# Kernel tuning notes

Hardware: AMD Instinct MI355X
Metric: run time of the kernel (lower is better)

## Reference

```python
import jax, jax.numpy as jnp
import numpy as np

B = 1024            # batch
F = (16, 16, 16)    # factors (f1, f2, f3)
BOND = 32           # bond dimension
SIZE = 4096         # prod(F)


def setup_inputs() -> dict:
    key = jax.random.key(0)
    k0, k1, k2, k3 = jax.random.split(key, 4)
    x = jax.random.normal(k0, (B, SIZE), dtype=jnp.float32)
    # cores: (r_{k-1}, f_k, f_k, r_k), boundary ranks = 1, init scale 0.01 as in torch
    core0 = jax.random.normal(k1, (1, F[0], F[0], BOND), dtype=jnp.float32) * 0.01
    core1 = jax.random.normal(k2, (BOND, F[1], F[1], BOND), dtype=jnp.float32) * 0.01
    core2 = jax.random.normal(k3, (BOND, F[2], F[2], 1), dtype=jnp.float32) * 0.01
    bias = jnp.zeros((SIZE,), dtype=jnp.float32)
    return {"x": x, "core0": core0, "core1": core1, "core2": core2, "bias": bias}


def reference(x, core0, core1, core2, bias):
    # Batched MPO (tensor-train) matvec: y[b, i1 i2 i3] = sum_{j1 j2 j3, r1 r2}
    #   G0[1, i1, j1, r1] G1[r1, i2, j2, r2] G2[r2, i3, j3, 1] * x[b, j1 j2 j3]
    b = x.shape[0]
    t = x.reshape(b, F[0], F[1], F[2])                       # (B, j1, j2, j3)
    # contract j1 with core0 -> carry bond r, accumulate output index i1 at the end
    t = jnp.einsum('bjkl,aijr->brkli', t, core0)             # (B, r1, j2, j3, i1)
    # contract (r1, j2) with core1
    t = jnp.einsum('brkli,rmks->bslim', t, core1)            # (B, r2, j3, i1, i2)
    # contract (r2, j3) with core2 (right bond t has size 1)
    y = jnp.einsum('bslim,snlt->bimnt', t, core2)            # (B, i1, i2, i3, 1)
    return y.reshape(b, SIZE) + bias
```

## Files before the change

### kernel.cpp

```cpp
#include <hip/hip_runtime.h>
#include <stdint.h>

typedef float f32x4_t __attribute__((ext_vector_type(4)));
typedef __bf16 bf16x8_t __attribute__((ext_vector_type(8)));

#define GLD16(gp, lp) __builtin_amdgcn_global_load_lds( \
    (const __attribute__((address_space(1))) void*)(gp), \
    (__attribute__((address_space(3))) void*)(lp), 16, 0, 0)

__device__ __forceinline__ uint32_t f2bf(float f) {
  uint32_t u = __float_as_uint(f);
  u += 0x7FFFu + ((u >> 16) & 1u);
  return u >> 16;
}
__device__ __forceinline__ uint32_t pack2(float a, float b) {
  return f2bf(a) | (f2bf(b) << 16);
}

__global__ __launch_bounds__(256) void build_m01_kernel(
    const float* __restrict__ c0, const float* __restrict__ c1,
    float* __restrict__ M01) {
  const int a = blockIdx.x, t = threadIdx.x;
  const int i1 = a >> 4, i2 = a & 15, j1 = t >> 4, j2 = t & 15;
  const float* c0p = c0 + (i1 * 16 + j1) * 32;
  const float4* c1v = (const float4*)(c1 + i2 * 512 + j2 * 32);

  float acc[32];
  #pragma unroll
  for (int r2 = 0; r2 < 32; ++r2) acc[r2] = 0.f;

  #pragma unroll 4
  for (int r1 = 0; r1 < 32; ++r1) {
    const float g = c0p[r1];
    #pragma unroll
    for (int q = 0; q < 8; ++q) {
      const float4 v = c1v[r1 * 2048 + q];
      acc[q * 4 + 0] += g * v.x; acc[q * 4 + 1] += g * v.y;
      acc[q * 4 + 2] += g * v.z; acc[q * 4 + 3] += g * v.w;
    }
  }
  float4* dst = (float4*)(M01 + (size_t)a * 8192 + t * 32);
  #pragma unroll
  for (int q = 0; q < 8; ++q) {
    float4 v = {acc[q * 4 + 0], acc[q * 4 + 1], acc[q * 4 + 2], acc[q * 4 + 3]};
    dst[q] = v;
  }
}

__global__ __launch_bounds__(256) void build_w2_kernel(
    const float* __restrict__ M01, const float* __restrict__ c2,
    uint16_t* __restrict__ W) {
  __shared__ float C2L[32 * 16];
  const int bid = blockIdx.x;
  const int a = bid >> 4, i3 = bid & 15, t = threadIdx.x;

  if (t < 128) {
    ((float4*)C2L)[t] = ((const float4*)c2)[(t >> 2) * 64 + i3 * 4 + (t & 3)];
  }
  __syncthreads();

  float M[32];
  const float4* mp = (const float4*)(M01 + (size_t)a * 8192 + t * 32);
  #pragma unroll
  for (int q = 0; q < 8; ++q) {
    const float4 v = mp[q];
    M[q * 4 + 0] = v.x; M[q * 4 + 1] = v.y; M[q * 4 + 2] = v.z; M[q * 4 + 3] = v.w;
  }

  float acc[16];
  #pragma unroll
  for (int j = 0; j < 16; ++j) acc[j] = 0.f;

  #pragma unroll 4
  for (int r2 = 0; r2 < 32; ++r2) {
    const float4* cp = (const float4*)(C2L + r2 * 16);
    const float4 q0 = cp[0], q1 = cp[1], q2 = cp[2], q3 = cp[3];
    const float m = M[r2];
    acc[0]  += m * q0.x; acc[1]  += m * q0.y; acc[2]  += m * q0.z; acc[3]  += m * q0.w;
    acc[4]  += m * q1.x; acc[5]  += m * q1.y; acc[6]  += m * q1.z; acc[7]  += m * q1.w;
    acc[8]  += m * q2.x; acc[9]  += m * q2.y; acc[10] += m * q2.z; acc[11] += m * q2.w;
    acc[12] += m * q3.x; acc[13] += m * q3.y; acc[14] += m * q3.z; acc[15] += m * q3.w;
  }

  uint4 o0, o1;
  o0.x = pack2(acc[0],  acc[1]);  o0.y = pack2(acc[2],  acc[3]);
  o0.z = pack2(acc[4],  acc[5]);  o0.w = pack2(acc[6],  acc[7]);
  o1.x = pack2(acc[8],  acc[9]);  o1.y = pack2(acc[10], acc[11]);
  o1.z = pack2(acc[12], acc[13]); o1.w = pack2(acc[14], acc[15]);
  uint4* dst = (uint4*)(W + (size_t)(a * 16 + i3) * 4096 + t * 16);
  dst[0] = o0; dst[1] = o1;
}

__global__ __launch_bounds__(256) void cvt_x_kernel(const float* __restrict__ x,
                                                    uint32_t* __restrict__ xb) {
  const int i = blockIdx.x * 256 + threadIdx.x;
  const float4* x4 = (const float4*)x;
  const float4 a = x4[2 * i], b = x4[2 * i + 1];
  uint4 o;
  o.x = pack2(a.x, a.y); o.y = pack2(a.z, a.w);
  o.z = pack2(b.x, b.y); o.w = pack2(b.z, b.w);
  ((uint4*)xb)[i] = o;
}

__global__ __launch_bounds__(256, 2) void gemm_bt_bias_kernel(
    const uint16_t* __restrict__ A, const uint16_t* __restrict__ Bt,
    const float* __restrict__ bias, float* __restrict__ C) {
  constexpr int Kd = 4096, Nd = 4096;
  __shared__ uint16_t As[2][64 * 64];
  __shared__ uint16_t Bs[2][128 * 64];
  const int t = threadIdx.x;
  const int wid = t >> 6, lane = t & 63;

  const int bid = blockIdx.x;
  const int g = bid & 7, idx = bid >> 3;
  const int ntile = g * 4 + (idx >> 4);
  const int mtile = idx & 15;
  const int brow = mtile * 64, bcol = ntile * 128;

  const uint16_t* Ab = A + (size_t)brow * Kd;
  const uint16_t* Bb = Bt + (size_t)bcol * Kd;

  const int rb = t >> 3;
  const int ce = ((t & 7) * 8) ^ ((rb & 7) << 3);
  const uint16_t* gA = Ab + (size_t)rb * Kd + ce;
  const uint16_t* gB = Bb + (size_t)rb * Kd + ce;
  const int wofs = wid * 512;

  const int wm = wid >> 1, wn = wid & 1;
  const int fr = lane & 15, fk = (lane >> 4) * 8;
  const int csw = (fr & 7) << 3;

  f32x4_t zero = {0.f, 0.f, 0.f, 0.f};
  f32x4_t acc[2][4];
  #pragma unroll
  for (int m = 0; m < 2; ++m)
    #pragma unroll
    for (int n = 0; n < 4; ++n) acc[m][n] = zero;

  #define STAGE(buf, kt)                                             \
    do {                                                             \
      GLD16(gA + (kt), As[buf] + wofs);                              \
      GLD16(gA + (size_t)32 * Kd + (kt), As[buf] + 2048 + wofs);     \
      GLD16(gB + (kt), Bs[buf] + wofs);                              \
      GLD16(gB + (size_t)32 * Kd + (kt), Bs[buf] + 2048 + wofs);     \
      GLD16(gB + (size_t)64 * Kd + (kt), Bs[buf] + 4096 + wofs);     \
      GLD16(gB + (size_t)96 * Kd + (kt), Bs[buf] + 6144 + wofs);     \
    } while (0)

  STAGE(0, 0);
  __syncthreads();

  int cur = 0;
  for (int kt = 0; kt < Kd; kt += 64) {
    if (kt + 64 < Kd) STAGE(cur ^ 1, kt + 64);

    bf16x8_t af[2][2], bfr[2][4];
    #pragma unroll
    for (int kk = 0; kk < 2; ++kk) {
      const int col = (kk * 32 + fk) ^ csw;
      #pragma unroll
      for (int m = 0; m < 2; ++m)
        af[kk][m] = *(const bf16x8_t*)(As[cur] + (wm * 32 + m * 16 + fr) * 64 + col);
      #pragma unroll
      for (int n = 0; n < 4; ++n)
        bfr[kk][n] = *(const bf16x8_t*)(Bs[cur] + (wn * 64 + n * 16 + fr) * 64 + col);
    }
    #pragma unroll
    for (int kk = 0; kk < 2; ++kk)
      #pragma unroll
      for (int m = 0; m < 2; ++m)
        #pragma unroll
        for (int n = 0; n < 4; ++n)
          acc[m][n] = __builtin_amdgcn_mfma_f32_16x16x32_bf16(
              af[kk][m], bfr[kk][n], acc[m][n], 0, 0, 0);

    __syncthreads();
    cur ^= 1;
  }
  #undef STAGE

  const int orow = brow + wm * 32 + (lane >> 4) * 4;
  const int ocol = bcol + wn * 64 + fr;
  #pragma unroll
  for (int n = 0; n < 4; ++n) {
    const float bv = bias[ocol + n * 16];
    #pragma unroll
    for (int m = 0; m < 2; ++m) {
      float* Cp = C + (size_t)(orow + m * 16) * Nd + ocol + n * 16;
      #pragma unroll
      for (int r = 0; r < 4; ++r) Cp[(size_t)r * Nd] = acc[m][n][r] + bv;
    }
  }
}

extern "C" void kernel_launch(void* const* d_in, const int* in_sizes, int n_in,
                              void* d_out, int out_size, void* d_ws, size_t ws_size,
                              hipStream_t stream) {
  const float* x    = (const float*)d_in[0];
  const float* c0   = (const float*)d_in[1];
  const float* c1   = (const float*)d_in[2];
  const float* c2   = (const float*)d_in[3];
  const float* bias = (const float*)d_in[4];
  float* y = (float*)d_out;

  uint16_t* W   = (uint16_t*)d_ws;
  char*     slab = (char*)d_ws + (size_t)4096 * 4096 * 2;
  float*    M01 = (float*)slab;
  uint16_t* xb  = (uint16_t*)slab;

  build_m01_kernel<<<256, 256, 0, stream>>>(c0, c1, M01);
  build_w2_kernel<<<4096, 256, 0, stream>>>(M01, c2, W);
  cvt_x_kernel<<<2048, 256, 0, stream>>>(x, (uint32_t*)xb);
  gemm_bt_bias_kernel<<<512, 256, 0, stream>>>(xb, W, bias, y);
}
```

Before: 192.0 us.

## Single-buffer GEMM LDS staging and batch four i3 slices per W-build block

The GEMM drops its double-buffered LDS pipeline. It now loads each K tile into a single buffer and waits on a barrier before the MFMAs, which halves LDS use and may raise occupancy, but it no longer overlaps global loads with compute. The W-build kernel now has each block handle four i3 slices, so M01 rows are read once per four outputs instead of once per output. Block indices are also remapped with an XCD-style interleave.

Result: faster. 182.4 us (-5.0%).

```diff
diff --git a/kernel.cpp b/kernel.cpp
--- a/kernel.cpp
+++ b/kernel.cpp
@@ -50,12 +50,19 @@
 __global__ __launch_bounds__(256) void build_w2_kernel(
     const float* __restrict__ M01, const float* __restrict__ c2,
     uint16_t* __restrict__ W) {
-  __shared__ float C2L[32 * 16];
-  const int bid = blockIdx.x;
-  const int a = bid >> 4, i3 = bid & 15, t = threadIdx.x;
-
-  if (t < 128) {
-    ((float4*)C2L)[t] = ((const float4*)c2)[(t >> 2) * 64 + i3 * 4 + (t & 3)];
+  __shared__ float C2L[4][512];
+  const int bid0 = blockIdx.x;
+  const int bid = (bid0 & 7) * 128 + (bid0 >> 3);
+  const int a = bid >> 2, i3q = (bid & 3) << 2;
+  const int t = threadIdx.x;
+
+  #pragma unroll
+  for (int s = 0; s < 2; ++s) {
+    const int idx = t * 2 + s;
+    const int sl = idx >> 7;
+    const int rem = idx & 127;
+    ((float4*)C2L[sl])[rem] =
+        ((const float4*)c2)[(rem >> 2) * 64 + (i3q + sl) * 4 + (rem & 3)];
   }
   __syncthreads();
 
@@ -67,28 +74,32 @@
     M[q * 4 + 0] = v.x; M[q * 4 + 1] = v.y; M[q * 4 + 2] = v.z; M[q * 4 + 3] = v.w;
   }
 
-  float acc[16];
-  #pragma unroll
-  for (int j = 0; j < 16; ++j) acc[j] = 0.f;
-
-  #pragma unroll 4
-  for (int r2 = 0; r2 < 32; ++r2) {
-    const float4* cp = (const float4*)(C2L + r2 * 16);
-    const float4 q0 = cp[0], q1 = cp[1], q2 = cp[2], q3 = cp[3];
-    const float m = M[r2];
-    acc[0]  += m * q0.x; acc[1]  += m * q0.y; acc[2]  += m * q0.z; acc[3]  += m * q0.w;
-    acc[4]  += m * q1.x; acc[5]  += m * q1.y; acc[6]  += m * q1.z; acc[7]  += m * q1.w;
-    acc[8]  += m * q2.x; acc[9]  += m * q2.y; acc[10] += m * q2.z; acc[11] += m * q2.w;
-    acc[12] += m * q3.x; acc[13] += m * q3.y; acc[14] += m * q3.z; acc[15] += m * q3.w;
-  }
-
-  uint4 o0, o1;
-  o0.x = pack2(acc[0],  acc[1]);  o0.y = pack2(acc[2],  acc[3]);
-  o0.z = pack2(acc[4],  acc[5]);  o0.w = pack2(acc[6],  acc[7]);
-  o1.x = pack2(acc[8],  acc[9]);  o1.y = pack2(acc[10], acc[11]);
-  o1.z = pack2(acc[12], acc[13]); o1.w = pack2(acc[14], acc[15]);
-  uint4* dst = (uint4*)(W + (size_t)(a * 16 + i3) * 4096 + t * 16);
-  dst[0] = o0; dst[1] = o1;
+  #pragma unroll 1
+  for (int i3l = 0; i3l < 4; ++i3l) {
+    float acc[16];
+    #pragma unroll
+    for (int j = 0; j < 16; ++j) acc[j] = 0.f;
+
+    const float* C2s = C2L[i3l];
+    #pragma unroll 4
+    for (int r2 = 0; r2 < 32; ++r2) {
+      const float4* cp = (const float4*)(C2s + r2 * 16);
+      const float4 q0 = cp[0], q1 = cp[1], q2 = cp[2], q3 = cp[3];
+      const float m = M[r2];
+      acc[0]  += m * q0.x; acc[1]  += m * q0.y; acc[2]  += m * q0.z; acc[3]  += m * q0.w;
+      acc[4]  += m * q1.x; acc[5]  += m * q1.y; acc[6]  += m * q1.z; acc[7]  += m * q1.w;
+      acc[8]  += m * q2.x; acc[9]  += m * q2.y; acc[10] += m * q2.z; acc[11] += m * q2.w;
+      acc[12] += m * q3.x; acc[13] += m * q3.y; acc[14] += m * q3.z; acc[15] += m * q3.w;
+    }
+
+    uint4 o0, o1;
+    o0.x = pack2(acc[0],  acc[1]);  o0.y = pack2(acc[2],  acc[3]);
+    o0.z = pack2(acc[4],  acc[5]);  o0.w = pack2(acc[6],  acc[7]);
+    o1.x = pack2(acc[8],  acc[9]);  o1.y = pack2(acc[10], acc[11]);
+    o1.z = pack2(acc[12], acc[13]); o1.w = pack2(acc[14], acc[15]);
+    uint4* dst = (uint4*)(W + (size_t)(a * 16 + i3q + i3l) * 4096 + t * 16);
+    dst[0] = o0; dst[1] = o1;
+  }
 }
 
 __global__ __launch_bounds__(256) void cvt_x_kernel(const float* __restrict__ x,
@@ -106,8 +117,8 @@
     const uint16_t* __restrict__ A, const uint16_t* __restrict__ Bt,
     const float* __restrict__ bias, float* __restrict__ C) {
   constexpr int Kd = 4096, Nd = 4096;
-  __shared__ uint16_t As[2][64 * 64];
-  __shared__ uint16_t Bs[2][128 * 64];
+  __shared__ uint16_t As[64 * 64];
+  __shared__ uint16_t Bs[128 * 64];
   const int t = threadIdx.x;
   const int wid = t >> 6, lane = t & 63;
 
@@ -124,7 +135,12 @@
   const int ce = ((t & 7) * 8) ^ ((rb & 7) << 3);
   const uint16_t* gA = Ab + (size_t)rb * Kd + ce;
   const uint16_t* gB = Bb + (size_t)rb * Kd + ce;
-  const int wofs = wid * 512;
+  uint16_t* lA0 = As + wid * 512;
+  uint16_t* lA1 = As + 2048 + wid * 512;
+  uint16_t* lB0 = Bs + wid * 512;
+  uint16_t* lB1 = Bs + 2048 + wid * 512;
+  uint16_t* lB2 = Bs + 4096 + wid * 512;
+  uint16_t* lB3 = Bs + 6144 + wid * 512;
 
   const int wm = wid >> 1, wn = wid & 1;
   const int fr = lane & 15, fk = (lane >> 4) * 8;
@@ -137,22 +153,14 @@
     #pragma unroll
     for (int n = 0; n < 4; ++n) acc[m][n] = zero;
 
-  #define STAGE(buf, kt)                                             \
-    do {                                                             \
-      GLD16(gA + (kt), As[buf] + wofs);                              \
-      GLD16(gA + (size_t)32 * Kd + (kt), As[buf] + 2048 + wofs);     \
-      GLD16(gB + (kt), Bs[buf] + wofs);                              \
-      GLD16(gB + (size_t)32 * Kd + (kt), Bs[buf] + 2048 + wofs);     \
-      GLD16(gB + (size_t)64 * Kd + (kt), Bs[buf] + 4096 + wofs);     \
-      GLD16(gB + (size_t)96 * Kd + (kt), Bs[buf] + 6144 + wofs);     \
-    } while (0)
-
-  STAGE(0, 0);
-  __syncthreads();
-
-  int cur = 0;
   for (int kt = 0; kt < Kd; kt += 64) {
-    if (kt + 64 < Kd) STAGE(cur ^ 1, kt + 64);
+    GLD16(gA + kt, lA0);
+    GLD16(gA + (size_t)32 * Kd + kt, lA1);
+    GLD16(gB + kt, lB0);
+    GLD16(gB + (size_t)32 * Kd + kt, lB1);
+    GLD16(gB + (size_t)64 * Kd + kt, lB2);
+    GLD16(gB + (size_t)96 * Kd + kt, lB3);
+    __syncthreads();
 
     bf16x8_t af[2][2], bfr[2][4];
     #pragma unroll
@@ -160,10 +168,10 @@
       const int col = (kk * 32 + fk) ^ csw;
       #pragma unroll
       for (int m = 0; m < 2; ++m)
-        af[kk][m] = *(const bf16x8_t*)(As[cur] + (wm * 32 + m * 16 + fr) * 64 + col);
+        af[kk][m] = *(const bf16x8_t*)(As + (wm * 32 + m * 16 + fr) * 64 + col);
       #pragma unroll
       for (int n = 0; n < 4; ++n)
-        bfr[kk][n] = *(const bf16x8_t*)(Bs[cur] + (wn * 64 + n * 16 + fr) * 64 + col);
+        bfr[kk][n] = *(const bf16x8_t*)(Bs + (wn * 64 + n * 16 + fr) * 64 + col);
     }
     #pragma unroll
     for (int kk = 0; kk < 2; ++kk)
@@ -173,11 +181,8 @@
         for (int n = 0; n < 4; ++n)
           acc[m][n] = __builtin_amdgcn_mfma_f32_16x16x32_bf16(
               af[kk][m], bfr[kk][n], acc[m][n], 0, 0, 0);
-
     __syncthreads();
-    cur ^= 1;
-  }
-  #undef STAGE
+  }
 
   const int orow = brow + wm * 32 + (lane >> 4) * 4;
   const int ocol = bcol + wn * 64 + fr;
@@ -203,13 +208,13 @@
   const float* bias = (const float*)d_in[4];
   float* y = (float*)d_out;
 
-  uint16_t* W   = (uint16_t*)d_ws;
+  uint16_t* W    = (uint16_t*)d_ws;
   char*     slab = (char*)d_ws + (size_t)4096 * 4096 * 2;
-  float*    M01 = (float*)slab;
-  uint16_t* xb  = (uint16_t*)slab;
+  float*    M01  = (float*)slab;
+  uint16_t* xb   = (uint16_t*)slab;
 
   build_m01_kernel<<<256, 256, 0, stream>>>(c0, c1, M01);
-  build_w2_kernel<<<4096, 256, 0, stream>>>(M01, c2, W);
+  build_w2_kernel<<<1024, 256, 0, stream>>>(M01, c2, W);
   cvt_x_kernel<<<2048, 256, 0, stream>>>(x, (uint32_t*)xb);
   gemm_bt_bias_kernel<<<512, 256, 0, stream>>>(xb, W, bias, y);
 }
```
